# Kernel tuning notes

Hardware: AMD Instinct MI355X
Metric: run time of the kernel (lower is better)

## Reference

```python
import jax, jax.numpy as jnp
import numpy as np

B, T_ENC, T_DEC, D, N_STATE = 32, 1024, 512, 512, 512


def setup_inputs() -> dict:
    key = jax.random.key(0)
    k1, k2, k3, k4 = jax.random.split(key, 4)
    scale = 1.0 / np.sqrt(D)
    return {
        "states_encoder": jax.random.normal(k1, (B, T_ENC, D), dtype=jnp.float32),
        "states_decoder": jax.random.normal(k2, (B, T_DEC, N_STATE), dtype=jnp.float32),
        "Wk": jax.random.normal(k3, (D, N_STATE), dtype=jnp.float32) * scale,
        "bk": jnp.zeros((N_STATE,), dtype=jnp.float32),
        "Wv": jax.random.normal(k4, (D, N_STATE), dtype=jnp.float32) * scale,
        "bv": jnp.zeros((N_STATE,), dtype=jnp.float32),
    }


def reference(states_encoder, states_decoder, Wk, bk, Wv, bv):
    # general Luong dot-product attention (n_state = int branch)
    key_vector = states_encoder @ Wk + bk          # [B, T_enc, N]
    val_vector = states_encoder @ Wv + bv          # [B, T_enc, N]
    # score[b, t_dec, t_enc] = sum_n dec[b,t_dec,n] * key[b,t_enc,n]
    score = jnp.einsum('bqn,bkn->bqk', states_decoder, key_vector)
    attention = jax.nn.softmax(score, axis=-1)     # over encoder positions
    # context[b, t_dec, n] = sum_k attention[b,t_dec,k] * val[b,k,n]
    context = jnp.einsum('bqk,bkn->bqn', attention, val_vector)
    return (context, attention)
```

## Files before the change

kernel.cpp:

```cpp
#include <hip/hip_runtime.h>
#include <math.h>

#define BB    32
#define TENC  1024
#define TDEC  512
#define DDIM  512
#define NST   512

typedef _Float16 f16_t;
typedef _Float16 f16x8 __attribute__((ext_vector_type(8)));
typedef _Float16 f16x4 __attribute__((ext_vector_type(4)));
typedef float    f32x4 __attribute__((ext_vector_type(4)));

#define GLOAD_LDS16(gp, lp) __builtin_amdgcn_global_load_lds( \
    (const __attribute__((address_space(1))) unsigned int*)(const void*)(gp), \
    (__attribute__((address_space(3))) unsigned int*)(lp), 16, 0, 0)

static __device__ __forceinline__ f32x4 MFMA16H(f16x8 a, f16x8 b, f32x4 c) {
    return __builtin_amdgcn_mfma_f32_16x16x32_f16(a, b, c, 0, 0, 0);
}

__global__ __launch_bounds__(256)
void prep_weights(const float* __restrict__ Wk, const float* __restrict__ Wv,
                  f16_t* __restrict__ Wk16, f16_t* __restrict__ WvT16)
{
    const int bid = blockIdx.x;
    const int t = threadIdx.x;

    if (bid < 128) {
        long i = (long)bid * 256 + t;
        float4 a = *(const float4*)&Wk[i * 8];
        float4 b = *(const float4*)&Wk[i * 8 + 4];
        f16x8 o;
        o[0] = (f16_t)a.x; o[1] = (f16_t)a.y; o[2] = (f16_t)a.z; o[3] = (f16_t)a.w;
        o[4] = (f16_t)b.x; o[5] = (f16_t)b.y; o[6] = (f16_t)b.z; o[7] = (f16_t)b.w;
        *(f16x8*)&Wk16[i * 8] = o;
        return;
    }

    __shared__ f16_t tile[64][65];
    const int r2 = bid - 128;
    const int c0 = (r2 & 7) * 64, r0 = (r2 >> 3) * 64;
    const int rr = t >> 4;
    const int cc = (t & 15) * 4;
#pragma unroll
    for (int p = 0; p < 4; ++p) {
        int r = rr + p * 16;
        float4 v = *(const float4*)&Wv[(long)(r0 + r) * NST + c0 + cc];
        tile[r][cc + 0] = (f16_t)v.x;
        tile[r][cc + 1] = (f16_t)v.y;
        tile[r][cc + 2] = (f16_t)v.z;
        tile[r][cc + 3] = (f16_t)v.w;
    }
    __syncthreads();
    const int dr = t >> 2;
    const int tc = (t & 3) * 16;
    f16_t tmp[16];
#pragma unroll
    for (int e = 0; e < 16; ++e) tmp[e] = tile[tc + e][dr];
    *(f16x8*)&WvT16[(long)(c0 + dr) * DDIM + r0 + tc]     = *(f16x8*)&tmp[0];
    *(f16x8*)&WvT16[(long)(c0 + dr) * DDIM + r0 + tc + 8] = *(f16x8*)&tmp[8];
}

template<int AREG, int EPI>
__global__ __launch_bounds__(256)
void gemm_rs(const float* __restrict__ Rf, const f16_t* __restrict__ Gh,
             const float* __restrict__ bias, void* __restrict__ C0,
             int M, int N, int K, long sRf, long sG, long sC)
{
    __shared__ f16_t lds[2][8192];

    const int tid  = threadIdx.x;
    const int wave = tid >> 6;
    const int lane = tid & 63;

    const int gx = gridDim.x, gy = gridDim.y;
    const long nwg = (long)gx * gy * gridDim.z;
    const long fo  = ((long)blockIdx.z * gy + blockIdx.y) * gx + blockIdx.x;
    const long f2 = (fo & 7) * (nwg >> 3) + (fo >> 3);
    const int bx  = (int)(f2 % gx);
    const int by  = (int)((f2 / gx) % gy);
    const long bz = f2 / ((long)gx * gy);

    const float* RfB = Rf + bz * sRf;
    const f16_t* GhB = Gh + bz * sG;

    const int row0 = by * 128;
    const int col0 = bx * 128;
    const int rbase = AREG ? row0 : col0;
    const int gbase = AREG ? col0 : row0;
    constexpr int rOff = AREG ? 0 : 4096;
    constexpr int gOff = AREG ? 4096 : 0;

    const int srow  = wave * 16 + (lane >> 2);
    const int sslot = (lane & 3) ^ ((srow >> 1) & 3);
    const int wdst  = wave * 512;

    const int rrow = tid >> 3;
    const int rk4  = (tid & 7) * 4;
    const int rgr  = rk4 >> 3;
    const int rh4  = rk4 & 4;

    const int fr = lane & 15;
    const int q  = lane >> 4;
    const int wr = (wave >> 1) * 64;
    const int wc = (wave & 1) * 64;
    int aro[4], bro[4];
#pragma unroll
    for (int i = 0; i < 4; ++i) {
        const int r = wr + i * 16 + fr;
        aro[i] = r * 32 + ((q ^ ((r >> 1) & 3)) * 8);
    }
#pragma unroll
    for (int j = 0; j < 4; ++j) {
        const int r = wc + j * 16 + fr;
        bro[j] = r * 32 + ((q ^ ((r >> 1) & 3)) * 8);
    }

    f32x4 acc[4][4] = {};
    float4 rS[4];
    f16x8 aH[4], bH[4];
    const int NT = K >> 5;

    auto stageG = [&](f16_t* buf, int kt) {
#pragma unroll
        for (int c = 0; c < 2; ++c) {
            const long go = (long)(gbase + c * 64 + srow) * K + kt + sslot * 8;
            GLOAD_LDS16(GhB + go, &buf[gOff + c * 2048 + wdst]);
        }
    };
    auto loadR = [&](int kt) {
#pragma unroll
        for (int i = 0; i < 4; ++i)
            rS[i] = *(const float4*)&RfB[(long)(rbase + i * 32 + rrow) * K + kt + rk4];
    };
    auto writeR = [&](f16_t* buf) {
#pragma unroll
        for (int i = 0; i < 4; ++i) {
            const int row = i * 32 + rrow;
            const int eo  = row * 32 + ((rgr ^ ((row >> 1) & 3)) * 8) + rh4;
            f16x4 h4;
            h4[0] = (f16_t)rS[i].x; h4[1] = (f16_t)rS[i].y;
            h4[2] = (f16_t)rS[i].z; h4[3] = (f16_t)rS[i].w;
            *(f16x4*)&buf[rOff + eo] = h4;
        }
    };
    auto readF = [&](const f16_t* buf) {
#pragma unroll
        for (int i = 0; i < 4; ++i) aH[i] = *(const f16x8*)&buf[aro[i]];
#pragma unroll
        for (int j = 0; j < 4; ++j) bH[j] = *(const f16x8*)&buf[4096 + bro[j]];
    };

    loadR(0);
    stageG(lds[0], 0);
    writeR(lds[0]);
    loadR(32);
    asm volatile("s_waitcnt vmcnt(4)" ::: "memory");
    asm volatile("s_waitcnt lgkmcnt(0)" ::: "memory");
    __builtin_amdgcn_s_barrier();
    readF(lds[0]);
    asm volatile("s_waitcnt lgkmcnt(0)" ::: "memory");
    __builtin_amdgcn_s_barrier();

    for (int t = 0; t < NT; ++t) {
        f16_t* nxt = lds[(t & 1) ^ 1];
        const bool pf = (t + 1 < NT);

        if (pf) {
            writeR(nxt);
            stageG(nxt, (t + 1) << 5);
            if (t + 2 < NT) loadR((t + 2) << 5);
        }
#pragma unroll
        for (int j = 0; j < 4; ++j)
#pragma unroll
            for (int i = 0; i < 4; ++i)
                acc[i][j] = MFMA16H(aH[i], bH[j], acc[i][j]);

        if (pf && (t + 2 < NT))
            asm volatile("s_waitcnt vmcnt(4)" ::: "memory");
        else
            asm volatile("s_waitcnt vmcnt(0)" ::: "memory");
        asm volatile("s_waitcnt lgkmcnt(0)" ::: "memory");
        __builtin_amdgcn_s_barrier();
        if (pf) {
            readF(nxt);
            asm volatile("s_waitcnt lgkmcnt(0)" ::: "memory");
        }
        __builtin_amdgcn_s_barrier();
    }

    const int frow = q * 4;
#pragma unroll
    for (int i = 0; i < 4; ++i) {
        const int rgl = row0 + wr + i * 16 + frow;
#pragma unroll
        for (int j = 0; j < 4; ++j) {
            const int cg = col0 + wc + j * 16 + fr;
            if constexpr (EPI == 2) {
                f16_t* C = (f16_t*)C0 + bz * sC;
#pragma unroll
                for (int r = 0; r < 4; ++r)
                    C[(long)(rgl + r) * N + cg] = (f16_t)acc[i][j][r];
            } else if constexpr (EPI == 0) {
                float* C = (float*)C0 + bz * sC;
#pragma unroll
                for (int r = 0; r < 4; ++r)
                    C[(long)(rgl + r) * N + cg] = acc[i][j][r];
            } else {
                float* C = (float*)C0 + bz * sC;
                const float badd = bias[cg];
#pragma unroll
                for (int r = 0; r < 4; ++r)
                    C[(long)(rgl + r) * N + cg] = acc[i][j][r] + badd;
            }
        }
    }
}

__global__ __launch_bounds__(256)
void softmax_rows(float* __restrict__ S)
{
    const long row = (long)blockIdx.x * 4 + (threadIdx.x >> 6);
    const int lane = threadIdx.x & 63;
    float* p = S + row * (long)TENC;

    float4 v[4];
    float m = -INFINITY;
#pragma unroll
    for (int i = 0; i < 4; ++i) {
        v[i] = *(const float4*)&p[i * 256 + lane * 4];
        m = fmaxf(fmaxf(fmaxf(v[i].x, v[i].y), fmaxf(v[i].z, v[i].w)), m);
    }
#pragma unroll
    for (int o = 32; o; o >>= 1) m = fmaxf(m, __shfl_xor(m, o, 64));

    float s = 0.f;
#pragma unroll
    for (int i = 0; i < 4; ++i) {
        v[i].x = __expf(v[i].x - m);
        v[i].y = __expf(v[i].y - m);
        v[i].z = __expf(v[i].z - m);
        v[i].w = __expf(v[i].w - m);
        s += v[i].x + v[i].y + v[i].z + v[i].w;
    }
#pragma unroll
    for (int o = 32; o; o >>= 1) s += __shfl_xor(s, o, 64);

    const float inv = 1.0f / s;
#pragma unroll
    for (int i = 0; i < 4; ++i) {
        v[i].x *= inv; v[i].y *= inv; v[i].z *= inv; v[i].w *= inv;
        *(float4*)&p[i * 256 + lane * 4] = v[i];
    }
}

#define TILE_M 64
#define TILE_N 64
#define TILE_K 16
template<bool B_TRANS, bool ADD_BIAS>
__global__ __launch_bounds__(256)
void gemm_f32(const float* __restrict__ A, const float* __restrict__ Bm,
              const float* __restrict__ bias, float* __restrict__ C,
              int M, int N, int K, int lda, int ldb,
              long strideA, long strideB, long strideC)
{
    __shared__ float As[TILE_K][TILE_M + 4];
    __shared__ float Bs[TILE_K][TILE_N + 4];
    const int b = blockIdx.z;
    A += (long)b * strideA; Bm += (long)b * strideB; C += (long)b * strideC;
    const int tid = threadIdx.x;
    const int tx = tid & 15, ty = tid >> 4;
    const int row0 = blockIdx.y * TILE_M, col0 = blockIdx.x * TILE_N;
    const int am = tid >> 2, ak = (tid & 3) * 4;
    float acc[4][4] = {};
    for (int kt = 0; kt < K; kt += TILE_K) {
        float4 a4 = *(const float4*)&A[(long)(row0 + am) * lda + kt + ak];
        float4 b4;
        if (B_TRANS) b4 = *(const float4*)&Bm[(long)(col0 + am) * ldb + kt + ak];
        else {
            const int bk_ = tid >> 4, bn = (tid & 15) * 4;
            b4 = *(const float4*)&Bm[(long)(kt + bk_) * ldb + col0 + bn];
        }
        __syncthreads();
        As[ak + 0][am] = a4.x; As[ak + 1][am] = a4.y;
        As[ak + 2][am] = a4.z; As[ak + 3][am] = a4.w;
        if (B_TRANS) {
            Bs[ak + 0][am] = b4.x; Bs[ak + 1][am] = b4.y;
            Bs[ak + 2][am] = b4.z; Bs[ak + 3][am] = b4.w;
        } else {
            const int bk_ = tid >> 4, bn = (tid & 15) * 4;
            *(float4*)&Bs[bk_][bn] = b4;
        }
        __syncthreads();
#pragma unroll
        for (int k = 0; k < TILE_K; ++k) {
            float4 av = *(const float4*)&As[k][ty * 4];
            float4 bv4 = *(const float4*)&Bs[k][tx * 4];
            float ar[4] = {av.x, av.y, av.z, av.w};
            float br[4] = {bv4.x, bv4.y, bv4.z, bv4.w};
#pragma unroll
            for (int i = 0; i < 4; ++i)
#pragma unroll
                for (int j = 0; j < 4; ++j)
                    acc[i][j] = fmaf(ar[i], br[j], acc[i][j]);
        }
    }
    float4 bias4 = make_float4(0.f, 0.f, 0.f, 0.f);
    if (ADD_BIAS) bias4 = *(const float4*)&bias[col0 + tx * 4];
#pragma unroll
    for (int i = 0; i < 4; ++i) {
        float4 o;
        o.x = acc[i][0] + bias4.x; o.y = acc[i][1] + bias4.y;
        o.z = acc[i][2] + bias4.z; o.w = acc[i][3] + bias4.w;
        *(float4*)&C[(long)(row0 + ty * 4 + i) * N + col0 + tx * 4] = o;
    }
}

extern "C" void kernel_launch(void* const* d_in, const int* in_sizes, int n_in,
                              void* d_out, int out_size, void* d_ws, size_t ws_size,
                              hipStream_t stream)
{
    const float* enc = (const float*)d_in[0];
    const float* dec = (const float*)d_in[1];
    const float* Wk  = (const float*)d_in[2];
    const float* Wv  = (const float*)d_in[4];
    const float* bv  = (const float*)d_in[5];

    const long nD = (long)BB * TDEC * NST;

    float* ctx   = (float*)d_out;
    float* attnF = ctx + nD;

    const size_t need = 35127296;
    const dim3 blk(256);

    if (ws_size < need) {
        float* ws = (float*)d_ws;
        gemm_f32<true, false><<<dim3(DDIM / 64, (BB * TDEC) / 64, 1), blk, 0, stream>>>(
            dec, Wk, nullptr, ws, BB * TDEC, DDIM, NST, NST, NST, 0, 0, 0);
        gemm_f32<true, false><<<dim3(TENC / 64, TDEC / 64, BB), blk, 0, stream>>>(
            ws, enc, nullptr, attnF, TDEC, TENC, DDIM, DDIM, DDIM,
            (long)TDEC * DDIM, (long)TENC * DDIM, (long)TDEC * TENC);
        softmax_rows<<<(BB * TDEC) / 4, blk, 0, stream>>>(attnF);
        gemm_f32<false, false><<<dim3(DDIM / 64, TDEC / 64, BB), blk, 0, stream>>>(
            attnF, enc, nullptr, ws, TDEC, DDIM, TENC, TENC, DDIM,
            (long)TDEC * TENC, (long)TENC * DDIM, (long)TDEC * DDIM);
        gemm_f32<false, true><<<dim3(NST / 64, (BB * TDEC) / 64, 1), blk, 0, stream>>>(
            ws, Wv, bv, ctx, BB * TDEC, NST, DDIM, DDIM, NST, 0, 0, 0);
        return;
    }

    char* w = (char*)d_ws;
    f16_t* EVT   = (f16_t*)(w);
    f16_t* Wk16  = (f16_t*)(w + 33554432);
    f16_t* WvT16 = (f16_t*)(w + 34078720);

    f16_t* DK16  = (f16_t*)ctx;

    prep_weights<<<192, blk, 0, stream>>>(Wk, Wv, Wk16, WvT16);

    gemm_rs<1, 2><<<dim3(DDIM / 128, (BB * TDEC) / 128, 1), blk, 0, stream>>>(
        dec, Wk16, nullptr, DK16,
        BB * TDEC, DDIM, NST, 0, 0, 0);

    gemm_rs<0, 2><<<dim3(TENC / 128, NST / 128, BB), blk, 0, stream>>>(
        enc, WvT16, nullptr, EVT,
        NST, TENC, DDIM,
        (long)TENC * DDIM, 0, (long)NST * TENC);

    gemm_rs<0, 0><<<dim3(TENC / 128, TDEC / 128, BB), blk, 0, stream>>>(
        enc, DK16, nullptr, attnF,
        TDEC, TENC, DDIM,
        (long)TENC * DDIM, (long)TDEC * DDIM, (long)TDEC * TENC);

    softmax_rows<<<(BB * TDEC) / 4, blk, 0, stream>>>(attnF);

    gemm_rs<1, 3><<<dim3(NST / 128, TDEC / 128, BB), blk, 0, stream>>>(
        attnF, EVT, bv, ctx,
        TDEC, NST, TENC,
        (long)TDEC * TENC, (long)NST * TENC, (long)TDEC * NST);
}
```

Measured before the change: 161.2 us.

## Pre-convert encoder states to fp16 once and use pure-fp16 GEMMs

Encoder states are converted to fp16 once in the prep kernel. The value projection and score GEMM then run through a new all-fp16 GEMM that stages both operands with direct global-to-LDS loads, instead of each reading and converting the fp32 encoder separately. The value projection is now a single large GEMM followed by an fp16 transpose kernel that produces the layout the context GEMM needs. This adds a conversion pass, a transpose launch and more workspace in exchange for less fp32 traffic and conversion work inside the GEMMs.

```diff
diff --git a/kernel.cpp b/kernel.cpp
--- a/kernel.cpp
+++ b/kernel.cpp
@@ -21,25 +21,29 @@
 }
 
 __global__ __launch_bounds__(256)
-void prep_weights(const float* __restrict__ Wk, const float* __restrict__ Wv,
-                  f16_t* __restrict__ Wk16, f16_t* __restrict__ WvT16)
+void prep_convert(const float* __restrict__ enc, const float* __restrict__ Wk,
+                  const float* __restrict__ Wv,
+                  f16_t* __restrict__ Ef16, f16_t* __restrict__ Wk16,
+                  f16_t* __restrict__ WvT16)
 {
     const int bid = blockIdx.x;
     const int t = threadIdx.x;
 
-    if (bid < 128) {
-        long i = (long)bid * 256 + t;
-        float4 a = *(const float4*)&Wk[i * 8];
-        float4 b = *(const float4*)&Wk[i * 8 + 4];
+    if (bid < 8320) {
+        const float* src; f16_t* dst; long i;
+        if (bid < 8192) { src = enc; dst = Ef16; i = (long)bid * 256 + t; }
+        else            { src = Wk;  dst = Wk16; i = (long)(bid - 8192) * 256 + t; }
+        float4 a = *(const float4*)&src[i * 8];
+        float4 b = *(const float4*)&src[i * 8 + 4];
         f16x8 o;
         o[0] = (f16_t)a.x; o[1] = (f16_t)a.y; o[2] = (f16_t)a.z; o[3] = (f16_t)a.w;
         o[4] = (f16_t)b.x; o[5] = (f16_t)b.y; o[6] = (f16_t)b.z; o[7] = (f16_t)b.w;
-        *(f16x8*)&Wk16[i * 8] = o;
+        *(f16x8*)&dst[i * 8] = o;
         return;
     }
 
     __shared__ f16_t tile[64][65];
-    const int r2 = bid - 128;
+    const int r2 = bid - 8320;
     const int c0 = (r2 & 7) * 64, r0 = (r2 >> 3) * 64;
     const int rr = t >> 4;
     const int cc = (t & 15) * 4;
@@ -62,11 +66,39 @@
     *(f16x8*)&WvT16[(long)(c0 + dr) * DDIM + r0 + tc + 8] = *(f16x8*)&tmp[8];
 }
 
-template<int AREG, int EPI>
 __global__ __launch_bounds__(256)
-void gemm_rs(const float* __restrict__ Rf, const f16_t* __restrict__ Gh,
-             const float* __restrict__ bias, void* __restrict__ C0,
-             int M, int N, int K, long sRf, long sG, long sC)
+void transpose_f16(const f16_t* __restrict__ in, f16_t* __restrict__ out,
+                   int R, int C, long sIn, long sOut)
+{
+    __shared__ f16_t tile[64][65];
+    const long b = blockIdx.z;
+    in  += b * sIn;
+    out += b * sOut;
+    const int r0 = blockIdx.x * 64;
+    const int c0 = blockIdx.y * 64;
+    const int t = threadIdx.x;
+    const int rr = t >> 4;
+    const int cc = (t & 15) * 4;
+#pragma unroll
+    for (int p = 0; p < 4; ++p) {
+        const int r = rr + p * 16;
+        *(f16x4*)&tile[r][cc] = *(const f16x4*)&in[(long)(r0 + r) * C + c0 + cc];
+    }
+    __syncthreads();
+    const int dr = t >> 2;
+    const int tc = (t & 3) * 16;
+    f16_t tmp[16];
+#pragma unroll
+    for (int e = 0; e < 16; ++e) tmp[e] = tile[tc + e][dr];
+    *(f16x8*)&out[(long)(c0 + dr) * R + r0 + tc]     = *(f16x8*)&tmp[0];
+    *(f16x8*)&out[(long)(c0 + dr) * R + r0 + tc + 8] = *(f16x8*)&tmp[8];
+}
+
+template<int EPI>
+__global__ __launch_bounds__(256)
+void gemm_h(const f16_t* __restrict__ A, const f16_t* __restrict__ B,
+            void* __restrict__ C0,
+            int M, int N, int K, long sA, long sB, long sC)
 {
     __shared__ f16_t lds[2][8192];
 
@@ -82,24 +114,19 @@
     const int by  = (int)((f2 / gx) % gy);
     const long bz = f2 / ((long)gx * gy);
 
-    const float* RfB = Rf + bz * sRf;
-    const f16_t* GhB = Gh + bz * sG;
+    const f16_t* Ab = A + bz * sA;
+    const f16_t* Bb = B + bz * sB;
 
     const int row0 = by * 128;
     const int col0 = bx * 128;
-    const int rbase = AREG ? row0 : col0;
-    const int gbase = AREG ? col0 : row0;
-    constexpr int rOff = AREG ? 0 : 4096;
-    constexpr int gOff = AREG ? 4096 : 0;
 
     const int srow  = wave * 16 + (lane >> 2);
     const int sslot = (lane & 3) ^ ((srow >> 1) & 3);
     const int wdst  = wave * 512;
-
-    const int rrow = tid >> 3;
-    const int rk4  = (tid & 7) * 4;
-    const int rgr  = rk4 >> 3;
-    const int rh4  = rk4 & 4;
+    const long aOff0 = (long)(row0 + srow) * K + sslot * 8;
+    const long aOff1 = (long)(row0 + 64 + srow) * K + sslot * 8;
+    const long bOff0 = (long)(col0 + srow) * K + sslot * 8;
+    const long bOff1 = (long)(col0 + 64 + srow) * K + sslot * 8;
 
     const int fr = lane & 15;
     const int q  = lane >> 4;
@@ -118,6 +145,121 @@
     }
 
     f32x4 acc[4][4] = {};
+    const int NT = K >> 5;
+
+#define STAGE(buf, kt) do {                                   \
+        GLOAD_LDS16(Ab + aOff0 + (kt), &(buf)[wdst]);         \
+        GLOAD_LDS16(Ab + aOff1 + (kt), &(buf)[2048 + wdst]);  \
+        GLOAD_LDS16(Bb + bOff0 + (kt), &(buf)[4096 + wdst]);  \
+        GLOAD_LDS16(Bb + bOff1 + (kt), &(buf)[6144 + wdst]);  \
+    } while (0)
+
+    STAGE(lds[0], 0);
+
+    for (int t = 0; t < NT; ++t) {
+        const f16_t* cur = lds[t & 1];
+        f16_t* nxt = lds[(t & 1) ^ 1];
+        const bool pf = (t + 1 < NT);
+
+        __builtin_amdgcn_sched_barrier(0);
+        __builtin_amdgcn_s_barrier();
+        if (pf) {
+            STAGE(nxt, (t + 1) << 5);
+            asm volatile("s_waitcnt vmcnt(4)" ::: "memory");
+        } else {
+            asm volatile("s_waitcnt vmcnt(0)" ::: "memory");
+        }
+        __builtin_amdgcn_s_barrier();
+        __builtin_amdgcn_sched_barrier(0);
+
+        f16x8 aH[4], bH[4];
+#pragma unroll
+        for (int i = 0; i < 4; ++i) aH[i] = *(const f16x8*)&cur[aro[i]];
+#pragma unroll
+        for (int j = 0; j < 4; ++j) bH[j] = *(const f16x8*)&cur[4096 + bro[j]];
+
+#pragma unroll
+        for (int j = 0; j < 4; ++j)
+#pragma unroll
+            for (int i = 0; i < 4; ++i)
+                acc[i][j] = MFMA16H(aH[i], bH[j], acc[i][j]);
+    }
+#undef STAGE
+
+    const int frow = q * 4;
+#pragma unroll
+    for (int i = 0; i < 4; ++i) {
+        const int rgl = row0 + wr + i * 16 + frow;
+#pragma unroll
+        for (int j = 0; j < 4; ++j) {
+            const int cg = col0 + wc + j * 16 + fr;
+            if constexpr (EPI == 2) {
+                f16_t* C = (f16_t*)C0 + bz * sC;
+#pragma unroll
+                for (int r = 0; r < 4; ++r)
+                    C[(long)(rgl + r) * N + cg] = (f16_t)acc[i][j][r];
+            } else {
+                float* C = (float*)C0 + bz * sC;
+#pragma unroll
+                for (int r = 0; r < 4; ++r)
+                    C[(long)(rgl + r) * N + cg] = acc[i][j][r];
+            }
+        }
+    }
+}
+
+template<int EPI>
+__global__ __launch_bounds__(256)
+void gemm_rs(const float* __restrict__ Rf, const f16_t* __restrict__ Gh,
+             const float* __restrict__ bias, void* __restrict__ C0,
+             int M, int N, int K, long sRf, long sG, long sC)
+{
+    __shared__ f16_t lds[2][8192];
+
+    const int tid  = threadIdx.x;
+    const int wave = tid >> 6;
+    const int lane = tid & 63;
+
+    const int gx = gridDim.x, gy = gridDim.y;
+    const long nwg = (long)gx * gy * gridDim.z;
+    const long fo  = ((long)blockIdx.z * gy + blockIdx.y) * gx + blockIdx.x;
+    const long f2 = (fo & 7) * (nwg >> 3) + (fo >> 3);
+    const int bx  = (int)(f2 % gx);
+    const int by  = (int)((f2 / gx) % gy);
+    const long bz = f2 / ((long)gx * gy);
+
+    const float* RfB = Rf + bz * sRf;
+    const f16_t* GhB = Gh + bz * sG;
+
+    const int row0 = by * 128;
+    const int col0 = bx * 128;
+
+    const int srow  = wave * 16 + (lane >> 2);
+    const int sslot = (lane & 3) ^ ((srow >> 1) & 3);
+    const int wdst  = wave * 512;
+
+    const int rrow = tid >> 3;
+    const int rk4  = (tid & 7) * 4;
+    const int rgr  = rk4 >> 3;
+    const int rh4  = rk4 & 4;
+
+    const int fr = lane & 15;
+    const int q  = lane >> 4;
+    const int wr = (wave >> 1) * 64;
+    const int wc = (wave & 1) * 64;
+    int aro[4], bro[4];
+#pragma unroll
+    for (int i = 0; i < 4; ++i) {
+        const int r = wr + i * 16 + fr;
+        aro[i] = r * 32 + ((q ^ ((r >> 1) & 3)) * 8);
+    }
+#pragma unroll
+    for (int j = 0; j < 4; ++j) {
+        const int r = wc + j * 16 + fr;
+        bro[j] = r * 32 + ((q ^ ((r >> 1) & 3)) * 8);
+    }
+
+    f32x4 acc[4][4] = {};
     float4 rS[4];
     f16x8 aH[4], bH[4];
     const int NT = K >> 5;
@@ -125,14 +267,14 @@
     auto stageG = [&](f16_t* buf, int kt) {
 #pragma unroll
         for (int c = 0; c < 2; ++c) {
-            const long go = (long)(gbase + c * 64 + srow) * K + kt + sslot * 8;
-            GLOAD_LDS16(GhB + go, &buf[gOff + c * 2048 + wdst]);
+            const long go = (long)(col0 + c * 64 + srow) * K + kt + sslot * 8;
+            GLOAD_LDS16(GhB + go, &buf[4096 + c * 2048 + wdst]);
         }
     };
     auto loadR = [&](int kt) {
 #pragma unroll
         for (int i = 0; i < 4; ++i)
-            rS[i] = *(const float4*)&RfB[(long)(rbase + i * 32 + rrow) * K + kt + rk4];
+            rS[i] = *(const float4*)&RfB[(long)(row0 + i * 32 + rrow) * K + kt + rk4];
     };
     auto writeR = [&](f16_t* buf) {
 #pragma unroll
@@ -142,7 +284,7 @@
             f16x4 h4;
             h4[0] = (f16_t)rS[i].x; h4[1] = (f16_t)rS[i].y;
             h4[2] = (f16_t)rS[i].z; h4[3] = (f16_t)rS[i].w;
-            *(f16x4*)&buf[rOff + eo] = h4;
+            *(f16x4*)&buf[eo] = h4;
         }
     };
     auto readF = [&](const f16_t* buf) {
@@ -203,11 +345,6 @@
 #pragma unroll
                 for (int r = 0; r < 4; ++r)
                     C[(long)(rgl + r) * N + cg] = (f16_t)acc[i][j][r];
-            } else if constexpr (EPI == 0) {
-                float* C = (float*)C0 + bz * sC;
-#pragma unroll
-                for (int r = 0; r < 4; ++r)
-                    C[(long)(rgl + r) * N + cg] = acc[i][j][r];
             } else {
                 float* C = (float*)C0 + bz * sC;
                 const float badd = bias[cg];
@@ -333,7 +470,7 @@
     float* ctx   = (float*)d_out;
     float* attnF = ctx + nD;
 
-    const size_t need = 35127296;
+    const size_t need = 68157440;
     const dim3 blk(256);
 
     if (ws_size < need) {
@@ -354,30 +491,34 @@
 
     char* w = (char*)d_ws;
     f16_t* EVT   = (f16_t*)(w);
-    f16_t* Wk16  = (f16_t*)(w + 33554432);
-    f16_t* WvT16 = (f16_t*)(w + 34078720);
-
-    f16_t* DK16  = (f16_t*)ctx;
-
-    prep_weights<<<192, blk, 0, stream>>>(Wk, Wv, Wk16, WvT16);
-
-    gemm_rs<1, 2><<<dim3(DDIM / 128, (BB * TDEC) / 128, 1), blk, 0, stream>>>(
+    f16_t* Ef16  = (f16_t*)(w + 33554432);
+    f16_t* Wk16  = (f16_t*)(w + 67108864);
+    f16_t* WvT16 = (f16_t*)(w + 67633152);
+
+    f16_t* DK16 = (f16_t*)ctx;
+    f16_t* EV   = (f16_t*)attnF;
+
+    prep_convert<<<8384, blk, 0, stream>>>(enc, Wk, Wv, Ef16, Wk16, WvT16);
+
+    gemm_rs<2><<<dim3(DDIM / 128, (BB * TDEC) / 128, 1), blk, 0, stream>>>(
         dec, Wk16, nullptr, DK16,
         BB * TDEC, DDIM, NST, 0, 0, 0);
 
-    gemm_rs<0, 2><<<dim3(TENC / 128, NST / 128, BB), blk, 0, stream>>>(
-        enc, WvT16, nullptr, EVT,
-        NST, TENC, DDIM,
-        (long)TENC * DDIM, 0, (long)NST * TENC);
-
-    gemm_rs<0, 0><<<dim3(TENC / 128, TDEC / 128, BB), blk, 0, stream>>>(
-        enc, DK16, nullptr, attnF,
+    gemm_h<2><<<dim3(NST / 128, (BB * TENC) / 128, 1), blk, 0, stream>>>(
+        Ef16, WvT16, EV,
+        BB * TENC, NST, DDIM, 0, 0, 0);
+
+    transpose_f16<<<dim3(TENC / 64, NST / 64, BB), blk, 0, stream>>>(
+        EV, EVT, TENC, NST, (long)TENC * NST, (long)NST * TENC);
+
+    gemm_h<0><<<dim3(TENC / 128, TDEC / 128, BB), blk, 0, stream>>>(
+        DK16, Ef16, attnF,
         TDEC, TENC, DDIM,
-        (long)TENC * DDIM, (long)TDEC * DDIM, (long)TDEC * TENC);
+        (long)TDEC * DDIM, (long)TENC * DDIM, (long)TDEC * TENC);
 
     softmax_rows<<<(BB * TDEC) / 4, blk, 0, stream>>>(attnF);
 
-    gemm_rs<1, 3><<<dim3(NST / 128, TDEC / 128, BB), blk, 0, stream>>>(
+    gemm_rs<3><<<dim3(NST / 128, TDEC / 128, BB), blk, 0, stream>>>(
         attnF, EVT, bv, ctx,
         TDEC, NST, TENC,
         (long)TDEC * TENC, (long)NST * TENC, (long)TDEC * NST);
```

Result: slower. 173.5 us (+7.6%).
